# Kernel optimization log

Hardware: AMD Instinct MI355X
Metric: run time of the kernel (lower is better)

## Reference

```python
import jax, jax.numpy as jnp
import numpy as np

WINDOW = 11
PAD = WINDOW // 2
C1 = 0.01 ** 2
C2 = 0.03 ** 2


def _avg_pool(x):
    # Matches torch F.avg_pool2d(x, k, stride=1, padding=k//2) with
    # count_include_pad=True (default): sum over zero-padded window / k^2.
    # Separable box filter: sum over H then W.
    s = jax.lax.reduce_window(
        x, 0.0, jax.lax.add,
        window_dimensions=(1, 1, WINDOW, 1), window_strides=(1, 1, 1, 1),
        padding=((0, 0), (0, 0), (PAD, PAD), (0, 0)))
    s = jax.lax.reduce_window(
        s, 0.0, jax.lax.add,
        window_dimensions=(1, 1, 1, WINDOW), window_strides=(1, 1, 1, 1),
        padding=((0, 0), (0, 0), (0, 0), (PAD, PAD)))
    return s * (1.0 / (WINDOW * WINDOW))


def setup_inputs() -> dict:
    key = jax.random.key(0)
    k1, k2 = jax.random.split(key)
    shape = (16, 3, 512, 512)
    pred = jax.random.uniform(k1, shape, dtype=jnp.float32)
    target = jax.random.uniform(k2, shape, dtype=jnp.float32)
    return {"pred": pred, "target": target}


def reference(pred, target):
    mu_x = _avg_pool(pred)
    mu_y = _avg_pool(target)
    mu_x_sq = mu_x * mu_x
    mu_y_sq = mu_y * mu_y
    mu_xy = mu_x * mu_y
    sigma_x = _avg_pool(pred * pred) - mu_x_sq
    sigma_y = _avg_pool(target * target) - mu_y_sq
    sigma_xy = _avg_pool(pred * target) - mu_xy
    ssim_map = ((2.0 * mu_xy + C1) * (2.0 * sigma_xy + C2)
                / ((mu_x_sq + mu_y_sq + C1) * (sigma_x + sigma_y + C2)))
    ssim_map = jnp.clip(ssim_map, 0.0, 1.0)
    # per-sample loss: 1 - mean over C,H,W
    return 1.0 - jnp.mean(ssim_map.reshape(ssim_map.shape[0], -1), axis=1)
```

## Files before the change

### kernel.cpp

```cpp
#include <hip/hip_runtime.h>
#include <hip/hip_fp16.h>

#define HH 512
#define WW 512
#define NCH 3
#define NBATCH 16
#define NIMG (NBATCH*NCH)
#define CHUNK 32
#define NCHUNK (HH/CHUNK)
#define NSTRIP 4
#define SW 128
#define SLOTS 140
#define NT 64
#define NROWS (CHUNK+10)
#define BLKS_PER_B (NCH*NCHUNK*NSTRIP)

struct RowData { float4 m; float2 h; };
union RingQ { float4 f; __half2 h[4]; };

__global__ __launch_bounds__(NT) void ssim_main(
    const float* __restrict__ pred, const float* __restrict__ targ,
    float* __restrict__ ws)
{
  __shared__ __align__(16) float2 rowb[SLOTS];
  __shared__ __align__(16) float4 ring[11][NT];

  const int l = threadIdx.x;
  const int blk = blockIdx.x;
  const int img = blk >> 6;
  const int rem = blk & 63;
  const int chunk = rem >> 2;
  const int strip = rem & 3;

  const int r0 = chunk*CHUNK - 5;
  const int c0 = strip*SW;

  if (l < 10) rowb[(l < 5) ? l : (128 + l)] = make_float2(0.f, 0.f);

  const size_t ib = (size_t)img * (size_t)(HH*WW);
  const float* pp = pred + ib;
  const float* tp = targ + ib;

  const int cm = c0 + 2*l;
  const int h  = l - 54;
  const int ch = (h < 5) ? (c0 - 5 + h) : (c0 + 123 + h);
  const bool hval = (l >= 54) && ((unsigned)ch < (unsigned)WW);
  const int hs = (h < 5) ? h : (128 + h);

  auto loadrow = [&](int it) -> RowData {
    RowData d;
    const int r = r0 + it;
    if ((unsigned)r < (unsigned)HH) {
      const size_t ro = (size_t)r * WW;
      const float2 x = *(const float2*)(pp + ro + cm);
      const float2 y = *(const float2*)(tp + ro + cm);
      d.m = make_float4(x.x, x.y, y.x, y.y);
      if (hval) d.h = make_float2(pp[ro + ch], tp[ro + ch]);
      else      d.h = make_float2(0.f, 0.f);
    } else {
      d.m = make_float4(0.f, 0.f, 0.f, 0.f);
      d.h = make_float2(0.f, 0.f);
    }
    return d;
  };

  float2 vx = make_float2(0.f,0.f), vy = vx, vxy = vx, vss = vx;
  float acc = 0.f;

  RowData cur = loadrow(0);
  RowData nxt = loadrow(1);
  RowData nx2 = loadrow(2);

  constexpr float c1 = 0.0001f, c2 = 0.0009f, inv121 = 1.0f/121.0f;

  auto ssim1 = [&](float Sx, float Sy, float Sxy, float Sss) -> float {
    const float mux = Sx*inv121, muy = Sy*inv121;
    const float muxy = mux*muy;
    const float m2   = fmaf(mux, mux, muy*muy);
    const float sgxy = fmaf(Sxy, inv121, -muxy);
    const float sgss = fmaf(Sss, inv121, -m2);
    const float num = fmaf(2.f, muxy, c1) * fmaf(2.f, sgxy, c2);
    const float den = (m2 + c1) * (sgss + c2);
    const float s = num * __builtin_amdgcn_rcpf(den);
    return fminf(fmaxf(s, 0.f), 1.f);
  };

  auto body = [&](int it, int slot, bool dosub, bool doemit) {
    rowb[5 + 2*l] = make_float2(cur.m.x, cur.m.z);
    rowb[6 + 2*l] = make_float2(cur.m.y, cur.m.w);
    if (hval) rowb[hs] = cur.h;
    cur = nxt; nxt = nx2;
    nx2 = loadrow(it + 3);

    const float4* tb = (const float4*)(rowb + 2*l);
    float4 tv[6];
    #pragma unroll
    for (int j = 0; j < 6; ++j) tv[j] = tb[j];

    RingQ ou;
    if (dosub) ou.f = ring[slot][l];

    float sx=0.f, sy=0.f, sxy=0.f, sss=0.f;
    float x0=0.f, y0=0.f, x11=0.f, y11=0.f;
    #pragma unroll
    for (int j = 0; j < 6; ++j) {
      const float4 v = tv[j];
      if (j == 0) { x0 = v.x; y0 = v.y; }
      sx += v.x; sy += v.y;
      sxy = fmaf(v.x, v.y, sxy);
      sss = fmaf(v.x, v.x, sss);
      sss = fmaf(v.y, v.y, sss);
      if (j < 5) {
        sx += v.z; sy += v.w;
        sxy = fmaf(v.z, v.w, sxy);
        sss = fmaf(v.z, v.z, sss);
        sss = fmaf(v.w, v.w, sss);
      } else { x11 = v.z; y11 = v.w; }
    }

    const float2 hx  = make_float2(sx,  sx - x0 + x11);
    const float2 hy  = make_float2(sy,  sy - y0 + y11);
    const float2 hxy = make_float2(sxy, fmaf(x11, y11, fmaf(-x0, y0, sxy)));
    const float2 hss = make_float2(sss,
        fmaf(x11, x11, fmaf(y11, y11, fmaf(-x0, x0, fmaf(-y0, y0, sss)))));

    RingQ qu;
    qu.h[0] = __floats2half2_rn(hx.x,  hy.x);
    qu.h[1] = __floats2half2_rn(hxy.x, hss.x);
    qu.h[2] = __floats2half2_rn(hx.y,  hy.y);
    qu.h[3] = __floats2half2_rn(hxy.y, hss.y);
    ring[slot][l] = qu.f;
    const float2 a0 = __half22float2(qu.h[0]), a1 = __half22float2(qu.h[1]);
    const float2 a2 = __half22float2(qu.h[2]), a3 = __half22float2(qu.h[3]);

    if (dosub) {
      const float2 oxy0 = __half22float2(ou.h[0]), ops0 = __half22float2(ou.h[1]);
      const float2 oxy1 = __half22float2(ou.h[2]), ops1 = __half22float2(ou.h[3]);
      vx.x  -= oxy0.x; vy.x  -= oxy0.y; vxy.x -= ops0.x; vss.x -= ops0.y;
      vx.y  -= oxy1.x; vy.y  -= oxy1.y; vxy.y -= ops1.x; vss.y -= ops1.y;
    }
    vx.x += a0.x; vy.x += a0.y; vxy.x += a1.x; vss.x += a1.y;
    vx.y += a2.x; vy.y += a2.y; vxy.y += a3.x; vss.y += a3.y;

    if (doemit) {
      acc += ssim1(vx.x, vy.x, vxy.x, vss.x);
      acc += ssim1(vx.y, vy.y, vxy.y, vss.y);
    }
  };

  #pragma unroll
  for (int u = 0; u < 11; ++u) body(u, u, false, u == 10);
  for (int g = 0; g < 2; ++g) {
    #pragma unroll
    for (int u = 0; u < 11; ++u) body(11 + 11*g + u, u, true, true);
  }
  #pragma unroll
  for (int u = 0; u < 9; ++u) body(33 + u, u, true, true);

  #pragma unroll
  for (int off = 32; off > 0; off >>= 1) acc += __shfl_down(acc, off, 64);
  if (l == 0) ws[blk] = acc;
}

__global__ void ssim_final(const float* __restrict__ ws, float* __restrict__ out) {
  const int b = blockIdx.x;
  const int t = threadIdx.x;
  const float* p = ws + b * BLKS_PER_B;
  float s = p[t] + p[t + 64] + p[t + 128];
  #pragma unroll
  for (int off = 32; off > 0; off >>= 1) s += __shfl_down(s, off, 64);
  if (t == 0) out[b] = 1.0f - s * (1.0f / (float)(NCH*HH*WW));
}

extern "C" void kernel_launch(void* const* d_in, const int* in_sizes, int n_in,
                              void* d_out, int out_size, void* d_ws, size_t ws_size,
                              hipStream_t stream) {
  const float* pred = (const float*)d_in[0];
  const float* targ = (const float*)d_in[1];
  float* out = (float*)d_out;
  float* ws  = (float*)d_ws;
  ssim_main<<<dim3(NIMG*NCHUNK*NSTRIP), dim3(NT), 0, stream>>>(pred, targ, ws);
  ssim_final<<<dim3(NBATCH), dim3(64), 0, stream>>>(ws, out);
}
```

Baseline: 148.7 us.

## Swap separable order: vertical running sums in registers from reloaded rows

```diff
diff --git a/kernel.cpp b/kernel.cpp
--- a/kernel.cpp
+++ b/kernel.cpp
@@ -1,5 +1,4 @@
 #include <hip/hip_runtime.h>
-#include <hip/hip_fp16.h>
 
 #define HH 512
 #define WW 512
@@ -10,20 +9,18 @@
 #define NCHUNK (HH/CHUNK)
 #define NSTRIP 4
 #define SW 128
-#define SLOTS 140
+#define SLOTS 142
 #define NT 64
-#define NROWS (CHUNK+10)
 #define BLKS_PER_B (NCH*NCHUNK*NSTRIP)
 
 struct RowData { float4 m; float2 h; };
-union RingQ { float4 f; __half2 h[4]; };
 
 __global__ __launch_bounds__(NT) void ssim_main(
     const float* __restrict__ pred, const float* __restrict__ targ,
     float* __restrict__ ws)
 {
-  __shared__ __align__(16) float2 rowb[SLOTS];
-  __shared__ __align__(16) float4 ring[11][NT];
+  __shared__ __align__(16) float2 arrA[SLOTS];
+  __shared__ __align__(16) float2 arrB[SLOTS];
 
   const int l = threadIdx.x;
   const int blk = blockIdx.x;
@@ -35,8 +32,6 @@
   const int r0 = chunk*CHUNK - 5;
   const int c0 = strip*SW;
 
-  if (l < 10) rowb[(l < 5) ? l : (128 + l)] = make_float2(0.f, 0.f);
-
   const size_t ib = (size_t)img * (size_t)(HH*WW);
   const float* pp = pred + ib;
   const float* tp = targ + ib;
@@ -45,7 +40,7 @@
   const int h  = l - 54;
   const int ch = (h < 5) ? (c0 - 5 + h) : (c0 + 123 + h);
   const bool hval = (l >= 54) && ((unsigned)ch < (unsigned)WW);
-  const int hs = (h < 5) ? h : (128 + h);
+  const int hs = (h < 5) ? (1 + h) : (129 + h);
 
   auto loadrow = [&](int it) -> RowData {
     RowData d;
@@ -64,12 +59,23 @@
     return d;
   };
 
-  float2 vx = make_float2(0.f,0.f), vy = vx, vxy = vx, vss = vx;
+  auto loadold = [&](int it) -> RowData {
+    if (it >= 0) return loadrow(it);
+    RowData d;
+    d.m = make_float4(0.f, 0.f, 0.f, 0.f);
+    d.h = make_float2(0.f, 0.f);
+    return d;
+  };
+
+  float vx0=0.f, vy0=0.f, vxy0=0.f, vss0=0.f;
+  float vx1=0.f, vy1=0.f, vxy1=0.f, vss1=0.f;
+  float vxh=0.f, vyh=0.f, vxyh=0.f, vssh=0.f;
   float acc = 0.f;
 
-  RowData cur = loadrow(0);
-  RowData nxt = loadrow(1);
-  RowData nx2 = loadrow(2);
+  RowData curN = loadrow(0);
+  RowData nxtN = loadrow(1);
+  RowData nx2N = loadrow(2);
+  RowData curO = loadold(-11);
 
   constexpr float c1 = 0.0001f, c2 = 0.0009f, inv121 = 1.0f/121.0f;
 
@@ -85,77 +91,72 @@
     return fminf(fmaxf(s, 0.f), 1.f);
   };
 
-  auto body = [&](int it, int slot, bool dosub, bool doemit) {
-    rowb[5 + 2*l] = make_float2(cur.m.x, cur.m.z);
-    rowb[6 + 2*l] = make_float2(cur.m.y, cur.m.w);
-    if (hval) rowb[hs] = cur.h;
-    cur = nxt; nxt = nx2;
-    nx2 = loadrow(it + 3);
-
-    const float4* tb = (const float4*)(rowb + 2*l);
-    float4 tv[6];
-    #pragma unroll
-    for (int j = 0; j < 6; ++j) tv[j] = tb[j];
-
-    RingQ ou;
-    if (dosub) ou.f = ring[slot][l];
-
-    float sx=0.f, sy=0.f, sxy=0.f, sss=0.f;
-    float x0=0.f, y0=0.f, x11=0.f, y11=0.f;
-    #pragma unroll
-    for (int j = 0; j < 6; ++j) {
-      const float4 v = tv[j];
-      if (j == 0) { x0 = v.x; y0 = v.y; }
-      sx += v.x; sy += v.y;
-      sxy = fmaf(v.x, v.y, sxy);
-      sss = fmaf(v.x, v.x, sss);
-      sss = fmaf(v.y, v.y, sss);
-      if (j < 5) {
-        sx += v.z; sy += v.w;
-        sxy = fmaf(v.z, v.w, sxy);
-        sss = fmaf(v.z, v.z, sss);
-        sss = fmaf(v.w, v.w, sss);
-      } else { x11 = v.z; y11 = v.w; }
+  auto body = [&](int it, bool doemit) {
+    {
+      const float xn0 = curN.m.x, xn1 = curN.m.y;
+      const float yn0 = curN.m.z, yn1 = curN.m.w;
+      const float xo0 = curO.m.x, xo1 = curO.m.y;
+      const float yo0 = curO.m.z, yo1 = curO.m.w;
+      vx0  += xn0 - xo0;  vy0  += yn0 - yo0;
+      vx1  += xn1 - xo1;  vy1  += yn1 - yo1;
+      vxy0 += xn0*yn0 - xo0*yo0;
+      vxy1 += xn1*yn1 - xo1*yo1;
+      vss0 += fmaf(xn0, xn0, yn0*yn0) - fmaf(xo0, xo0, yo0*yo0);
+      vss1 += fmaf(xn1, xn1, yn1*yn1) - fmaf(xo1, xo1, yo1*yo1);
+      const float xnh = curN.h.x, ynh = curN.h.y;
+      const float xoh = curO.h.x, yoh = curO.h.y;
+      vxh  += xnh - xoh;  vyh  += ynh - yoh;
+      vxyh += xnh*ynh - xoh*yoh;
+      vssh += fmaf(xnh, xnh, ynh*ynh) - fmaf(xoh, xoh, yoh*yoh);
     }
 
-    const float2 hx  = make_float2(sx,  sx - x0 + x11);
-    const float2 hy  = make_float2(sy,  sy - y0 + y11);
-    const float2 hxy = make_float2(sxy, fmaf(x11, y11, fmaf(-x0, y0, sxy)));
-    const float2 hss = make_float2(sss,
-        fmaf(x11, x11, fmaf(y11, y11, fmaf(-x0, x0, fmaf(-y0, y0, sss)))));
+    curN = nxtN; nxtN = nx2N;
+    nx2N = loadrow(it + 3);
+    RowData oN = loadold(it - 10);
 
-    RingQ qu;
-    qu.h[0] = __floats2half2_rn(hx.x,  hy.x);
-    qu.h[1] = __floats2half2_rn(hxy.x, hss.x);
-    qu.h[2] = __floats2half2_rn(hx.y,  hy.y);
-    qu.h[3] = __floats2half2_rn(hxy.y, hss.y);
-    ring[slot][l] = qu.f;
-    const float2 a0 = __half22float2(qu.h[0]), a1 = __half22float2(qu.h[1]);
-    const float2 a2 = __half22float2(qu.h[2]), a3 = __half22float2(qu.h[3]);
+    *(float4*)(arrA + 6 + 2*l) = make_float4(vx0, vy0, vx1, vy1);
+    *(float4*)(arrB + 6 + 2*l) = make_float4(vxy0, vss0, vxy1, vss1);
+    if (l >= 54) {
+      arrA[hs] = make_float2(vxh, vyh);
+      arrB[hs] = make_float2(vxyh, vssh);
+    }
 
-    if (dosub) {
-      const float2 oxy0 = __half22float2(ou.h[0]), ops0 = __half22float2(ou.h[1]);
-      const float2 oxy1 = __half22float2(ou.h[2]), ops1 = __half22float2(ou.h[3]);
-      vx.x  -= oxy0.x; vy.x  -= oxy0.y; vxy.x -= ops0.x; vss.x -= ops0.y;
-      vx.y  -= oxy1.x; vy.y  -= oxy1.y; vxy.y -= ops1.x; vss.y -= ops1.y;
-    }
-    vx.x += a0.x; vy.x += a0.y; vxy.x += a1.x; vss.x += a1.y;
-    vx.y += a2.x; vy.y += a2.y; vxy.y += a3.x; vss.y += a3.y;
+    const float4* ta = (const float4*)(arrA) + l;
+    const float4 a0v = ta[0], a1v = ta[1], a2v = ta[2], a3v = ta[3],
+                 a4v = ta[4], a5v = ta[5], a6v = ta[6];
+    const float4* tb = (const float4*)(arrB) + l;
+    const float4 b0v = tb[0], b1v = tb[1], b2v = tb[2], b3v = tb[3],
+                 b4v = tb[4], b5v = tb[5], b6v = tb[6];
+
+    float Sx = a0v.z, Sy = a0v.w;
+    Sx += a1v.x; Sy += a1v.y;  Sx += a1v.z; Sy += a1v.w;
+    Sx += a2v.x; Sy += a2v.y;  Sx += a2v.z; Sy += a2v.w;
+    Sx += a3v.x; Sy += a3v.y;  Sx += a3v.z; Sy += a3v.w;
+    Sx += a4v.x; Sy += a4v.y;  Sx += a4v.z; Sy += a4v.w;
+    Sx += a5v.x; Sy += a5v.y;  Sx += a5v.z; Sy += a5v.w;
+    const float Sx1 = Sx - a0v.z + a6v.x;
+    const float Sy1 = Sy - a0v.w + a6v.y;
+
+    float Sxy = b0v.z, Sss = b0v.w;
+    Sxy += b1v.x; Sss += b1v.y;  Sxy += b1v.z; Sss += b1v.w;
+    Sxy += b2v.x; Sss += b2v.y;  Sxy += b2v.z; Sss += b2v.w;
+    Sxy += b3v.x; Sss += b3v.y;  Sxy += b3v.z; Sss += b3v.w;
+    Sxy += b4v.x; Sss += b4v.y;  Sxy += b4v.z; Sss += b4v.w;
+    Sxy += b5v.x; Sss += b5v.y;  Sxy += b5v.z; Sss += b5v.w;
+    const float Sxy1 = Sxy - b0v.z + b6v.x;
+    const float Sss1 = Sss - b0v.w + b6v.y;
 
     if (doemit) {
-      acc += ssim1(vx.x, vy.x, vxy.x, vss.x);
-      acc += ssim1(vx.y, vy.y, vxy.y, vss.y);
+      acc += ssim1(Sx,  Sy,  Sxy,  Sss);
+      acc += ssim1(Sx1, Sy1, Sxy1, Sss1);
     }
+    curO = oN;
   };
 
-  #pragma unroll
-  for (int u = 0; u < 11; ++u) body(u, u, false, u == 10);
-  for (int g = 0; g < 2; ++g) {
-    #pragma unroll
-    for (int u = 0; u < 11; ++u) body(11 + 11*g + u, u, true, true);
-  }
-  #pragma unroll
-  for (int u = 0; u < 9; ++u) body(33 + u, u, true, true);
+  #pragma clang loop unroll_count(2)
+  for (int it = 0; it < 10; ++it) body(it, false);
+  #pragma clang loop unroll_count(2)
+  for (int it = 10; it < 42; ++it) body(it, true);
 
   #pragma unroll
   for (int off = 32; off > 0; off >>= 1) acc += __shfl_down(acc, off, 64);
```

Result: faster. 145.4 us (-2.3%).
